# Kernel optimization log

Hardware: AMD Instinct MI355X
Metric: run time of the kernel (lower is better)

The kernel has to match this reference:

```python
import jax, jax.numpy as jnp
import numpy as np
from jax import lax


def conv1x1(x, w, b):
    # x [B,Ci,H,W], w [Co,Ci], b [Co]
    return jnp.einsum('oi,bihw->bohw', w, x) + b[None, :, None, None]


def dil_conv_relu(x, w, b):
    # 3x3 conv, dilation 2, padding 2 (make_layers with dilation=True), then ReLU
    y = lax.conv_general_dilated(x, w, (1, 1), [(2, 2), (2, 2)], rhs_dilation=(2, 2),
                                 dimension_numbers=('NCHW', 'OIHW', 'NCHW'))
    return jax.nn.relu(y + b[None, :, None, None])


def conv1d_relu(x, w, b):
    # x [n,c,L], w [o,i,9], padding 4 -> same length; conv + ReLU (nn.Sequential(Conv2d, ReLU))
    y = lax.conv_general_dilated(x, w, (1,), [(4, 4)], dimension_numbers=('NCH', 'OIH', 'NCH'))
    return jax.nn.relu(y + b[None, :, None])


def dulr_pass(slices, w, b):
    # slices [L,n,c,m]; out[0]=slices[0]; out[i]=convrelu(out[i-1]) + slices[i]
    def step(carry, s):
        new = conv1d_relu(carry, w, b) + s
        return new, new
    _, rest = lax.scan(step, slices[0], slices[1:])
    return jnp.concatenate([slices[:1], rest], axis=0)


def conv_du(x, w, b):
    # down pass then up pass over rows (kernel (1,9) -> 1D conv along width)
    rows = jnp.moveaxis(x, 2, 0)            # [h,n,c,w]
    rows = dulr_pass(rows, w, b)
    rows = dulr_pass(rows[::-1], w, b)[::-1]
    return jnp.moveaxis(rows, 0, 2)


def conv_lr(x, w, b):
    # left-right then right-left over columns (kernel (9,1) -> 1D conv along height)
    cols = jnp.moveaxis(x, 3, 0)            # [w,n,c,h]
    cols = dulr_pass(cols, w, b)
    cols = dulr_pass(cols[::-1], w, b)[::-1]
    return jnp.moveaxis(cols, 0, 3)


def setup_inputs() -> dict:
    key = jax.random.key(0)
    ks = jax.random.split(key, 24)
    B, H, W = 4, 64, 64
    std = 0.01
    f32 = jnp.float32
    d = {}
    d['in_data'] = jax.random.normal(ks[0], (B, 1025, H, W), f32)
    d['wA'] = jax.random.normal(ks[1], (128, 1024), f32) * std
    d['bA'] = jax.random.normal(ks[2], (128,), f32) * std
    d['wB'] = jax.random.normal(ks[3], (128, 1024), f32) * std
    d['bB'] = jax.random.normal(ks[4], (128,), f32) * std
    d['wC'] = jax.random.normal(ks[5], (1024, 1024), f32) * std
    d['bC'] = jax.random.normal(ks[6], (1024,), f32) * std
    d['gamma'] = jnp.array(0.1, f32)
    chans = [(512, 1024), (512, 512), (512, 512), (256, 512), (128, 256), (64, 128)]
    for i, (co, ci) in enumerate(chans):
        d[f'bw{i+1}'] = jax.random.normal(ks[7 + 2 * i], (co, ci, 3, 3), f32) * std
        d[f'bb{i+1}'] = jax.random.normal(ks[8 + 2 * i], (co,), f32) * std
    d['du_w'] = jax.random.normal(ks[19], (64, 64, 9), f32) * std
    d['du_b'] = jax.random.normal(ks[20], (64,), f32) * std
    d['lr_w'] = jax.random.normal(ks[21], (64, 64, 9), f32) * std
    d['lr_b'] = jax.random.normal(ks[22], (64,), f32) * std
    d['ow'] = jax.random.normal(ks[23], (1, 64), f32) * std
    d['ob'] = jnp.zeros((1,), f32)
    return d


def reference(in_data, wA, bA, wB, bB, wC, bC, gamma,
              bw1, bb1, bw2, bb2, bw3, bb3, bw4, bb4, bw5, bb5, bw6, bb6,
              du_w, du_b, lr_w, lr_b, ow, ob):
    x = in_data[:, :1024]                   # [B,1024,H,W]
    f = in_data[:, 1024:1025]               # [B,1,H,W]
    B, C, H, W = x.shape
    N = H * W
    # appearance_A(x) -> query [B,128,N]
    q = conv1x1(x, wA, bA).reshape(B, 128, N)
    # f1024 = f broadcast to 1024 channels; flow_B(f1024) (1x1 conv) == f * sum_i wB[:,i] + bB
    k = (f * wB.sum(axis=1)[None, :, None, None] + bB[None, :, None, None]).reshape(B, 128, N)
    energy = jnp.einsum('bcn,bcm->bnm', q, k)           # [B,N,N] = q^T k
    att = jax.nn.softmax(energy, axis=-1)
    v = conv1x1(x, wC, bC).reshape(B, C, N)             # appearance_C
    out = jnp.einsum('bcj,bij->bci', v, att).reshape(B, C, H, W)  # bmm(v, att^T)
    x = gamma * out + x
    for w_, b_ in ((bw1, bb1), (bw2, bb2), (bw3, bb3), (bw4, bb4), (bw5, bb5), (bw6, bb6)):
        x = dil_conv_relu(x, w_, b_)
    x = conv_du(x, du_w, du_b)
    x = conv_lr(x, lr_w, lr_b)
    x = jax.nn.relu(conv1x1(x, ow, ob))                 # o_layer
    # F.upsample(scale_factor=8) default nearest
    x = jnp.repeat(jnp.repeat(x, 8, axis=2), 8, axis=3)
    return x
```

## Files before the change

kernel.cpp:

```cpp
#include <hip/hip_runtime.h>


#define NPIX 4096

typedef _Float16 f16;
typedef _Float16 f16x8 __attribute__((ext_vector_type(8)));
typedef _Float16 f16x4 __attribute__((ext_vector_type(4)));
typedef float f32x4 __attribute__((ext_vector_type(4)));

__device__ inline void async16(const void* g, void* l) {
  __builtin_amdgcn_global_load_lds(
      (const __attribute__((address_space(1))) unsigned int*)g,
      (__attribute__((address_space(3))) unsigned int*)l, 16, 0, 0);
}


__global__ void rf_zero(float* __restrict__ z) { z[threadIdx.x] = 0.f; }

__global__ void rf_s(const float* __restrict__ wB, const float* __restrict__ bA,
                     float* __restrict__ s_out, float* __restrict__ c0_out) {
  int c = threadIdx.x;
  const float* row = wB + (size_t)c * 1024;
  float acc = 0.f;
  for (int i = 0; i < 1024; ++i) acc += row[i];
  s_out[c] = acc;
  __shared__ float sh[128];
  sh[c] = acc * bA[c];
  __syncthreads();
  for (int off = 64; off > 0; off >>= 1) {
    if (c < off) sh[c] += sh[c + off];
    __syncthreads();
  }
  if (c == 0) c0_out[0] = sh[0];
}

__global__ void rf_u(const float* __restrict__ wA, const float* __restrict__ s,
                     float* __restrict__ u) {
  int i = blockIdx.x * 256 + threadIdx.x;
  float acc = 0.f;
  for (int c = 0; c < 128; ++c) acc += s[c] * wA[(size_t)c * 1024 + i];
  u[i] = acc;
}

__global__ void rf_fstat(const float* __restrict__ in, float* __restrict__ fstat) {
  int b = blockIdx.x;
  int t = threadIdx.x;
  const float* f = in + ((size_t)b * 1025 + 1024) * NPIX;
  float mx = -1e30f, mn = 1e30f;
  for (int j = t; j < NPIX; j += 256) {
    float v = f[j];
    mx = fmaxf(mx, v);
    mn = fminf(mn, v);
  }
  __shared__ float smx[256], smn[256];
  smx[t] = mx; smn[t] = mn;
  __syncthreads();
  for (int off = 128; off > 0; off >>= 1) {
    if (t < off) {
      smx[t] = fmaxf(smx[t], smx[t + off]);
      smn[t] = fminf(smn[t], smn[t + off]);
    }
    __syncthreads();
  }
  if (t == 0) { fstat[b] = smx[0]; fstat[4 + b] = smn[0]; }
}

__global__ __launch_bounds__(256) void rf_A(const float* __restrict__ in,
                                            const float* __restrict__ u,
                                            const float* __restrict__ c0p,
                                            const float* __restrict__ fst,
                                            float* __restrict__ A, float* __restrict__ M) {
  __shared__ float ul[1024];
  int b = blockIdx.y;
  int n = blockIdx.x * 256 + threadIdx.x;
  for (int s = threadIdx.x; s < 1024; s += 256) ul[s] = u[s];
  __syncthreads();
  const float* xp = in + (size_t)b * 1025 * NPIX + n;
  float acc = c0p[0];
#pragma unroll 8
  for (int i = 0; i < 1024; ++i) acc = fmaf(ul[i], xp[(size_t)i * NPIX], acc);
  A[b * NPIX + n] = acc;
  M[b * NPIX + n] = fmaxf(acc * fst[b], acc * fst[4 + b]);
}

__global__ void rf_Z(const float* __restrict__ in, const float* __restrict__ A,
                     const float* __restrict__ M, float* __restrict__ iZ) {
  int idx = blockIdx.x * 4 + (threadIdx.x >> 6);
  int lane = threadIdx.x & 63;
  int b = idx >> 12;
  const float* f = in + ((size_t)b * 1025 + 1024) * NPIX;
  float a = A[idx], m = M[idx];
  float acc = 0.f;
#pragma unroll 4
  for (int it = 0; it < 64; ++it) acc += __expf(a * f[lane + it * 64] - m);
  for (int off = 32; off > 0; off >>= 1) acc += __shfl_down(acc, off, 64);
  if (lane == 0) iZ[idx] = 1.0f / acc;
}


__global__ void rf_xsplit(const float* __restrict__ in, f16* __restrict__ xh) {
  __shared__ float tl[64][65];
  int nt = blockIdx.x, ct = blockIdx.y, b = blockIdx.z;
  int n0 = nt * 64, c0 = ct * 64;
  int tid = threadIdx.x;
  for (int s = tid; s < 4096; s += 256) {
    int r = s >> 6, c = s & 63;
    tl[r][c] = in[((size_t)b * 1025 + c0 + r) * NPIX + n0 + c];
  }
  __syncthreads();
  for (int s = tid; s < 512; s += 256) {
    int n = s >> 3, g = s & 7;
    f16x8 hb;
#pragma unroll
    for (int q = 0; q < 8; ++q) hb[q] = (f16)(16.f * tl[g * 8 + q][n]);
    size_t o = (((size_t)b * 128 + (c0 >> 3) + g) * 4096 + n0 + n) * 8;
    *(f16x8*)&xh[o] = hb;
  }
}


__global__ void rf_wC1(const float* __restrict__ wC, f16* __restrict__ wh) {
  int base = (blockIdx.x * 256 + threadIdx.x) * 8;
  int c = base >> 10, i0 = base & 1023;
  f16x8 hb;
#pragma unroll
  for (int q = 0; q < 8; ++q) hb[q] = (f16)(256.f * wC[base + q]);
  *(f16x8*)&wh[(((size_t)(i0 >> 3)) * 1024 + c) * 8] = hb;
}


__global__ __launch_bounds__(256, 2) void rf_vgemmm(
    const f16* __restrict__ wh, const f16* __restrict__ xh,
    const float* __restrict__ bC, f16* __restrict__ vH) {
  __shared__ f16 sA[2][4096], sB[2][4096];
  const int tid = threadIdx.x;
  const int nb = blockIdx.x * 128, cb = blockIdx.y * 128, b = blockIdx.z;
  const int pA = tid & 127;
  const int wv = tid >> 6, lane = tid & 63;
  const int mrow = lane & 15, quad = lane >> 4;
  const int wm = (wv & 1) * 64, wn = (wv >> 1) * 64;
  f32x4 acc[4][4];
#pragma unroll
  for (int i = 0; i < 4; ++i)
#pragma unroll
    for (int j = 0; j < 4; ++j) acc[i][j] = (f32x4){0.f, 0.f, 0.f, 0.f};

  auto stage = [&](int k0, int pb) {
    const int kg = k0 >> 3;
#pragma unroll
    for (int s = 0; s < 2; ++s) {
      const int cc = ((tid + 256 * s) >> 7) & 3;
      const int lb = ((tid & ~63) + 256 * s) * 8;
      async16(wh + ((size_t)(kg + cc) * 1024 + cb + pA) * 8, &sA[pb][lb]);
      async16(xh + (((size_t)b * 128 + kg + cc) * 4096 + nb + pA) * 8, &sB[pb][lb]);
    }
  };
  stage(0, 0);
  int p = 0;
  for (int k0 = 0; k0 < 1024; k0 += 32) {
    __syncthreads();
    if (k0 + 32 < 1024) stage(k0 + 32, p ^ 1);
    f16x8 fa[4], fb[4];
#pragma unroll
    for (int mi = 0; mi < 4; ++mi)
      fa[mi] = *(const f16x8*)&sA[p][(quad * 128 + wm + mi * 16 + mrow) * 8];
#pragma unroll
    for (int ni = 0; ni < 4; ++ni)
      fb[ni] = *(const f16x8*)&sB[p][(quad * 128 + wn + ni * 16 + mrow) * 8];
#pragma unroll
    for (int mi = 0; mi < 4; ++mi)
#pragma unroll
      for (int ni = 0; ni < 4; ++ni)
        acc[mi][ni] = __builtin_amdgcn_mfma_f32_16x16x32_f16(fa[mi], fb[ni], acc[mi][ni], 0, 0, 0);
    p ^= 1;
  }
  const float inv = 1.0f / 4096.0f;
#pragma unroll
  for (int mi = 0; mi < 4; ++mi) {
#pragma unroll
    for (int rg = 0; rg < 4; ++rg) {
      int c = cb + wm + mi * 16 + quad * 4 + rg;
      float bv = bC[c];
#pragma unroll
      for (int ni = 0; ni < 4; ++ni) {
        int j = nb + wn + ni * 16 + mrow;
        vH[(((size_t)b * 512 + (j >> 3)) * 1024 + c) * 8 + (j & 7)] =
            (f16)(16.f * (acc[mi][ni][rg] * inv + bv));
      }
    }
  }
}


__global__ __launch_bounds__(256, 2) void rf_attm(
    const f16* __restrict__ vH,
    const float* __restrict__ Aarr, const float* __restrict__ Marr,
    const float* __restrict__ iZ, const float* __restrict__ in,
    const float* __restrict__ gptr, f16* __restrict__ yH) {
  __shared__ f16 sAh[3][8192];
  __shared__ f16 sPh[2][4096];
  __shared__ float fl[4096];
  const int tid = threadIdx.x;
  const int ib = blockIdx.x * 128, cb = blockIdx.y * 256, b = blockIdx.z;
  const int wv = tid >> 6, lane = tid & 63;
  const int mrow = lane & 15, quad = lane >> 4;
  const int wm = wv * 64;
  const int ni_ = tid & 127;
  const int kc0 = tid >> 7;
  const float av2 = Aarr[b * NPIX + ib + ni_] * 1.44269504f;
  const float mv2 = Marr[b * NPIX + ib + ni_] * 1.44269504f;
  const float* f = in + ((size_t)b * 1025 + 1024) * NPIX;
  const f16* vbase = vH + (size_t)b * 4194304 + ((size_t)cb + tid) * 8;

  f32x4 acc[4][8];
#pragma unroll
  for (int i = 0; i < 4; ++i)
#pragma unroll
    for (int j = 0; j < 8; ++j) acc[i][j] = (f32x4){0.f, 0.f, 0.f, 0.f};

  auto stage = [&](int j0, int pb) {
    const int jg = j0 >> 3;
#pragma unroll
    for (int s = 0; s < 4; ++s)
      async16(vbase + (size_t)(jg + s) * 8192, &sAh[pb][(s * 256 + tid) * 8]);
  };
  auto doP = [&](int j0, int pb) {
#pragma unroll
    for (int it = 0; it < 2; ++it) {
      const int kc = kc0 + 2 * it;
      const float4 fa4 = *(const float4*)&fl[j0 + kc * 8];
      const float4 fb4 = *(const float4*)&fl[j0 + kc * 8 + 4];
      const float fj[8] = {fa4.x, fa4.y, fa4.z, fa4.w, fb4.x, fb4.y, fb4.z, fb4.w};
      f16x8 ph;
#pragma unroll
      for (int q = 0; q < 8; ++q)
        ph[q] = (f16)exp2f(fmaf(av2, fj[q], -mv2));
      *(f16x8*)&sPh[pb][(kc * 128 + ni_) * 8] = ph;
    }
  };

#pragma unroll
  for (int s = 0; s < 4; ++s)
    async16(f + (tid + 256 * s) * 4, &fl[((tid & ~63) + 256 * s) * 4]);
  stage(0, 0);
  asm volatile("s_waitcnt vmcnt(0)" ::: "memory");
  __builtin_amdgcn_s_barrier();
  doP(0, 0);
  stage(32, 1);
  asm volatile("s_waitcnt lgkmcnt(0)" ::: "memory");
  __builtin_amdgcn_s_barrier();

  for (int k = 0; k < 126; ++k) {
    const int pa = k % 3;
    const int pp = k & 1;
    f16x8 fa[4], fb[8];
#pragma unroll
    for (int mi = 0; mi < 4; ++mi)
      fa[mi] = *(const f16x8*)&sAh[pa][(quad * 256 + wm + mi * 16 + mrow) * 8];
#pragma unroll
    for (int ni = 0; ni < 8; ++ni)
      fb[ni] = *(const f16x8*)&sPh[pp][(quad * 128 + ni * 16 + mrow) * 8];
    stage((k + 2) * 32, (k + 2) % 3);
    doP((k + 1) * 32, pp ^ 1);
#pragma unroll
    for (int mi = 0; mi < 4; ++mi)
#pragma unroll
      for (int ni = 0; ni < 8; ++ni)
        acc[mi][ni] = __builtin_amdgcn_mfma_f32_16x16x32_f16(fa[mi], fb[ni], acc[mi][ni], 0, 0, 0);
    asm volatile("s_waitcnt vmcnt(4) lgkmcnt(0)" ::: "memory");
    __builtin_amdgcn_s_barrier();
  }
  {
    f16x8 fa[4], fb[8];
#pragma unroll
    for (int mi = 0; mi < 4; ++mi)
      fa[mi] = *(const f16x8*)&sAh[0][(quad * 256 + wm + mi * 16 + mrow) * 8];
#pragma unroll
    for (int ni = 0; ni < 8; ++ni)
      fb[ni] = *(const f16x8*)&sPh[0][(quad * 128 + ni * 16 + mrow) * 8];
    doP(127 * 32, 1);
#pragma unroll
    for (int mi = 0; mi < 4; ++mi)
#pragma unroll
      for (int ni = 0; ni < 8; ++ni)
        acc[mi][ni] = __builtin_amdgcn_mfma_f32_16x16x32_f16(fa[mi], fb[ni], acc[mi][ni], 0, 0, 0);
    asm volatile("s_waitcnt vmcnt(0) lgkmcnt(0)" ::: "memory");
    __builtin_amdgcn_s_barrier();
  }
  {
    f16x8 fa[4], fb[8];
#pragma unroll
    for (int mi = 0; mi < 4; ++mi)
      fa[mi] = *(const f16x8*)&sAh[1][(quad * 256 + wm + mi * 16 + mrow) * 8];
#pragma unroll
    for (int ni = 0; ni < 8; ++ni)
      fb[ni] = *(const f16x8*)&sPh[1][(quad * 128 + ni * 16 + mrow) * 8];
#pragma unroll
    for (int mi = 0; mi < 4; ++mi)
#pragma unroll
      for (int ni = 0; ni < 8; ++ni)
        acc[mi][ni] = __builtin_amdgcn_mfma_f32_16x16x32_f16(fa[mi], fb[ni], acc[mi][ni], 0, 0, 0);
  }

  const float g = gptr[0];
  const float inv16 = 1.0f / 16.0f;
  float zvi[8];
#pragma unroll
  for (int ni = 0; ni < 8; ++ni)
    zvi[ni] = iZ[b * NPIX + ib + ni * 16 + mrow] * inv16;
#pragma unroll
  for (int mi = 0; mi < 4; ++mi) {
    const int cbase = cb + wm + mi * 16 + quad * 4;
#pragma unroll
    for (int ni = 0; ni < 8; ++ni) {
      const int i = ib + ni * 16 + mrow;
      f16x4 hv;
#pragma unroll
      for (int rg = 0; rg < 4; ++rg) {
        float xr = in[((size_t)b * 1025 + cbase + rg) * NPIX + i];
        hv[rg] = (f16)(16.f * (g * (acc[mi][ni][rg] * zvi[ni]) + xr));
      }
      *(f16x4*)&yH[(((size_t)b * 128 + (cbase >> 3)) * 4096 + i) * 8 + (cbase & 7)] = hv;
    }
  }
}


__global__ void rf_wfragc(const float* __restrict__ w, f16* __restrict__ F,
                          int CI, int CO) {
  int gid = blockIdx.x * 256 + threadIdx.x;
  const int C16 = CO >> 4, KI = CI >> 5;
  const int total = 9 * KI * C16 * 64;
  if (gid >= total) return;
  int lane = gid & 63;
  int rest = gid >> 6;
  int c16 = rest % C16;
  int rest2 = rest / C16;
  int k = rest2 % KI;
  int t = rest2 / KI;
  int co = c16 * 16 + (lane & 15);
  int ci = k * 32 + (lane >> 4) * 8;
  f16x8 hb;
#pragma unroll
  for (int j = 0; j < 8; ++j)
    hb[j] = (f16)(256.0f * w[((size_t)co * CI + ci + j) * 9 + t]);
  *(f16x8*)&F[(size_t)gid * 8] = hb;
}


template <int BM, int BN, bool F32OUT>
__global__ __launch_bounds__(256, 2) void rf_mconv(
    const f16* __restrict__ xh, const f16* __restrict__ F,
    const float* __restrict__ bias, const float* __restrict__ zp,
    f16* __restrict__ oh, float* __restrict__ of, int CI, int CO) {
  constexpr int ROWS = BM / 64;
  constexpr int TPI = 4096 / BM;
  constexpr int HROWS = ROWS + 4;
  constexpr int COLP = 72;
  constexpr int CHUNKS = HROWS * 4 * COLP;
  constexpr int NSTG = (CHUNKS + 255) / 256;
  __shared__ f16 sA[2][NSTG * 2048];
  const int tid = threadIdx.x;
  const int blkpx = blockIdx.x;
  const int cob = blockIdx.y * BN;
  const int b = blkpx / TPI;
  const int h0 = (blkpx - b * TPI) * ROWS;

  const int wv = tid >> 6, lane = tid & 63;
  const int mrow = lane & 15, quad = lane >> 4;
  const int wm = (BN == 128) ? (wv & 1) * 64 : wv * 64;
  const int wn = (BN == 128) ? (wv >> 1) * 64 : 0;
  const int r_out = wm >> 6;
  const int KI = CI >> 5;
  const int C16 = CO >> 4;
  const int cb16 = (cob + wn) >> 4;

  f32x4 acc[4][4];
#pragma unroll
  for (int i = 0; i < 4; ++i)
#pragma unroll
    for (int j = 0; j < 4; ++j) acc[i][j] = (f32x4){0.f, 0.f, 0.f, 0.f};

  const f16* abase[NSTG];
  unsigned vmask = 0;
#pragma unroll
  for (int s = 0; s < NSTG; ++s) {
    int idx = tid + 256 * s;
    int rowks = idx / COLP;
    int col = idx - rowks * COLP;
    int r = rowks >> 2, ks = rowks & 3;
    int srow = h0 + r - 2, scol = col - 2;
    bool ok = (idx < CHUNKS) && ((unsigned)srow < 64u) && ((unsigned)scol < 64u);
    abase[s] = ok ? xh + (((size_t)b * (CI >> 3) + ks) * 4096 + srow * 64 + scol) * 8
                  : (const f16*)zp;
    if (ok) vmask |= (1u << s);
  }
  auto stageA = [&](int k, int pb) {
#pragma unroll
    for (int s = 0; s < NSTG; ++s) {
      const f16* sp = abase[s] + (((vmask >> s) & 1u) ? k * 131072 : 0);
      async16(sp, &sA[pb][((tid & ~63) + 256 * s) * 8]);
    }
  };

  const f16* Fb = F + ((size_t)cb16 * 64 + lane) * 8;
  auto loadFB = [&](f16x8* dst, int t, int k) {
#pragma unroll
    for (int ni = 0; ni < 4; ++ni)
      dst[ni] = *(const f16x8*)(Fb + ((size_t)(t * KI + k) * C16 + ni) * 512);
  };

  stageA(0, 0);
  f16x8 fb0[4], fb1[4];
  loadFB(fb0, 0, 0);

  for (int k2 = 0; k2 < KI; k2 += 2) {
#pragma unroll
    for (int dk = 0; dk < 2; ++dk) {
      const int k = k2 + dk;
      __syncthreads();
#pragma unroll
      for (int t = 0; t < 9; ++t) {
        const int par = (t + dk) & 1;
        f16x8* cur = par ? fb1 : fb0;
        f16x8* nxt = par ? fb0 : fb1;
        if (t < 8) loadFB(nxt, t + 1, k);
        else if (k + 1 < KI) loadFB(nxt, 0, k + 1);
        const int dh = (t / 3) * 2 - 2, dw = (t - (t / 3) * 3) * 2 - 2;
        f16x8 fa[4];
#pragma unroll
        for (int mi = 0; mi < 4; ++mi)
          fa[mi] = *(const f16x8*)&sA[dk][(((r_out + dh + 2) * 4 + quad) * COLP +
                                          mi * 16 + mrow + dw + 2) * 8];
#pragma unroll
        for (int mi = 0; mi < 4; ++mi)
#pragma unroll
          for (int ni = 0; ni < 4; ++ni)
            acc[mi][ni] = __builtin_amdgcn_mfma_f32_16x16x32_f16(fa[mi], cur[ni], acc[mi][ni], 0, 0, 0);
      }
      if (k + 1 < KI) stageA(k + 1, dk ^ 1);
    }
  }

  const float inv = 1.0f / 4096.0f;
  float bvs[4];
#pragma unroll
  for (int ni = 0; ni < 4; ++ni) bvs[ni] = bias[cob + wn + ni * 16 + mrow];
#pragma unroll
  for (int mi = 0; mi < 4; ++mi) {
#pragma unroll
    for (int rg = 0; rg < 4; ++rg) {
      int px = wm + mi * 16 + quad * 4 + rg;
      int hh = h0 + (px >> 6), wwp = px & 63;
#pragma unroll
      for (int ni = 0; ni < 4; ++ni) {
        int co = cob + wn + ni * 16 + mrow;
        float vv = fmaxf(acc[mi][ni][rg] * inv + bvs[ni], 0.f);
        if (F32OUT) {
          of[(((size_t)b * CO + co) * 64 + hh) * 64 + wwp] = vv;
        } else {
          oh[(((size_t)b * (CO >> 3) + (co >> 3)) * 4096 + hh * 64 + wwp) * 8 + (co & 7)] =
              (f16)(vv * 16.f);
        }
      }
    }
  }
}


__global__ void rf_wfrag(const float* __restrict__ w, f16* __restrict__ fh) {
  int gid = blockIdx.x * 256 + threadIdx.x;
  if (gid >= 4608) return;
  int lane = gid & 63;
  int rem = gid >> 6;
  int kc = rem & 1;
  int rem2 = rem >> 1;
  int t = rem2 % 9;
  int w4 = rem2 / 9;
  int co = w4 * 16 + (lane & 15);
  int cib = kc * 32 + (lane >> 4) * 8;
  f16x8 hb;
#pragma unroll
  for (int j = 0; j < 8; ++j)
    hb[j] = (f16)(256.f * w[((size_t)co * 64 + cib + j) * 9 + t]);
  *(f16x8*)&fh[(size_t)gid * 8] = hb;
}


__global__ __launch_bounds__(256, 1) void rf_mscan(
    const float* __restrict__ src, float* __restrict__ dst,
    const f16* __restrict__ fh, const float* __restrict__ bias, int dir) {
  __shared__ f16 ch[72 * 64];
  const int b = blockIdx.x;
  const int tid = threadIdx.x;
  const int wave = tid >> 6, lane = tid & 63;
  const int quad = lane >> 4, l15 = lane & 15;

  f16x8 Ah[9][2];
#pragma unroll
  for (int t = 0; t < 9; ++t)
#pragma unroll
    for (int kc = 0; kc < 2; ++kc)
      Ah[t][kc] = *(const f16x8*)&fh[(((wave * 9 + t) * 2 + kc) * 64 + lane) * 8];
  float bvs[4];
#pragma unroll
  for (int r = 0; r < 4; ++r) bvs[r] = bias[wave * 16 + quad * 4 + r];

  for (int s = tid; s < 2304; s += 256) ((unsigned*)ch)[s] = 0u;
  __syncthreads();

  const size_t sbase = (size_t)b * 64 * 4096;
  const int row0 = (dir > 0) ? 0 : 63;
  {
    int pos0 = tid & 63, cig = tid >> 6;
#pragma unroll
    for (int q = 0; q < 16; ++q) {
      int ci = cig * 16 + q;
      float v = src[sbase + (size_t)ci * 4096 + row0 * 64 + pos0];
      dst[sbase + (size_t)ci * 4096 + row0 * 64 + pos0] = v;
      int rowIdx = pos0 + 4;
      ch[rowIdx * 64 + (((ci >> 3) ^ (rowIdx & 7)) << 3) + (ci & 7)] = (f16)v;
    }
  }
  __syncthreads();

  const float inv = 1.0f / 256.0f;
  for (int s = 1; s < 64; ++s) {
    const int row = (dir > 0) ? s : 63 - s;
    float srow[4][4];
#pragma unroll
    for (int nt = 0; nt < 4; ++nt)
#pragma unroll
      for (int r = 0; r < 4; ++r)
        srow[nt][r] = src[sbase + (size_t)(wave * 16 + quad * 4 + r) * 4096 +
                          row * 64 + nt * 16 + l15];
    f32x4 acc[4];
#pragma unroll
    for (int nt = 0; nt < 4; ++nt) acc[nt] = (f32x4){0.f, 0.f, 0.f, 0.f};
#pragma unroll
    for (int t = 0; t < 9; ++t)
#pragma unroll
      for (int kc = 0; kc < 2; ++kc) {
#pragma unroll
        for (int nt = 0; nt < 4; ++nt) {
          int rowIdx = nt * 16 + l15 + t;
          int gr = kc * 4 + quad;
          f16x8 Bh = *(const f16x8*)&ch[rowIdx * 64 + ((gr ^ (rowIdx & 7)) << 3)];
          acc[nt] = __builtin_amdgcn_mfma_f32_16x16x32_f16(Ah[t][kc], Bh, acc[nt], 0, 0, 0);
        }
      }
    __syncthreads();
#pragma unroll
    for (int nt = 0; nt < 4; ++nt) {
      int pos = nt * 16 + l15;
      int rowIdx = pos + 4;
      f16x4 hv;
#pragma unroll
      for (int r = 0; r < 4; ++r) {
        float v = fmaxf(acc[nt][r] * inv + bvs[r], 0.f) + srow[nt][r];
        dst[sbase + (size_t)(wave * 16 + quad * 4 + r) * 4096 + row * 64 + pos] = v;
        hv[r] = (f16)v;
      }
      int ci0 = wave * 16 + quad * 4;
      *(f16x4*)&ch[rowIdx * 64 + (((ci0 >> 3) ^ (rowIdx & 7)) << 3) + (ci0 & 7)] = hv;
    }
    __syncthreads();
  }
}


__global__ void rf_transpose(const float* __restrict__ src, float* __restrict__ dst) {
  int bc = blockIdx.x;
  __shared__ float tl[64][65];
  int tid = threadIdx.x;
  const float* sp = src + (size_t)bc * 4096;
  float* dp = dst + (size_t)bc * 4096;
  for (int s = tid; s < 4096; s += 256) {
    int h = s >> 6, w = s & 63;
    tl[w][h] = sp[s];
  }
  __syncthreads();
  for (int s = tid; s < 4096; s += 256) dp[s] = tl[s >> 6][s & 63];
}


__global__ void rf_final(const float* __restrict__ t, const float* __restrict__ ow,
                         const float* __restrict__ ob, float* __restrict__ out) {
  int b = blockIdx.y;
  int s = blockIdx.x * 256 + threadIdx.x;
  int w = s >> 6, h = s & 63;
  float acc = ob[0];
  for (int c = 0; c < 64; ++c)
    acc += ow[c] * t[(((size_t)b * 64 + c) * 64 + w) * 64 + h];
  acc = fmaxf(acc, 0.f);
  float4 vv = make_float4(acc, acc, acc, acc);
  for (int dy = 0; dy < 8; ++dy) {
    float* dp = out + ((size_t)b * 512 + h * 8 + dy) * 512 + w * 8;
    *(float4*)dp = vv;
    *(float4*)(dp + 4) = vv;
  }
}


extern "C" void kernel_launch(void* const* d_in, const int* in_sizes, int n_in,
                              void* d_out, int out_size, void* d_ws, size_t ws_size,
                              hipStream_t stream) {
  const float* in    = (const float*)d_in[0];
  const float* wA    = (const float*)d_in[1];
  const float* bA    = (const float*)d_in[2];
  const float* wB    = (const float*)d_in[3];
  const float* wC    = (const float*)d_in[5];
  const float* bC    = (const float*)d_in[6];
  const float* gamma = (const float*)d_in[7];
  const float* bw1 = (const float*)d_in[8];  const float* bb1 = (const float*)d_in[9];
  const float* bw2 = (const float*)d_in[10]; const float* bb2 = (const float*)d_in[11];
  const float* bw3 = (const float*)d_in[12]; const float* bb3 = (const float*)d_in[13];
  const float* bw4 = (const float*)d_in[14]; const float* bb4 = (const float*)d_in[15];
  const float* bw5 = (const float*)d_in[16]; const float* bb5 = (const float*)d_in[17];
  const float* bw6 = (const float*)d_in[18]; const float* bb6 = (const float*)d_in[19];
  const float* du_w = (const float*)d_in[20]; const float* du_b = (const float*)d_in[21];
  const float* lr_w = (const float*)d_in[22]; const float* lr_b = (const float*)d_in[23];
  const float* ow   = (const float*)d_in[24]; const float* ob   = (const float*)d_in[25];
  float* out = (float*)d_out;
  float* ws = (float*)d_ws;

  f16* vH  = (f16*)(ws + 0);
  f16* xTh = (f16*)(ws + 4194304);
  f16* wCh = (f16*)(ws + 8388608);
  f16* yH  = (f16*)(ws + 16777216);
  f16* w1h = (f16*)(ws + 0);
  f16* c1H = (f16*)(ws + 2359296);
  f16* w3h = (f16*)(ws + 6553600);
  f16* w2h = (f16*)(ws + 16777216);
  f16* c2H = (f16*)(ws + 17956864);
  f16* w4h = (f16*)(ws + 22151168);
  f16* c4H = (f16*)(ws + 22740992);
  f16* c3H = c1H;
  f16* w5h = (f16*)(ws + 0);
  f16* c5H = (f16*)(ws + 147456);
  f16* w6h = (f16*)(ws + 1196032);
  float* tin = ws + 1232896;
  float* t0  = ws + 2281472;
  float* t1  = ws + 3330048;
  f16* duFh = (f16*)(ws + 4378624);
  f16* lrFh = (f16*)(ws + 4397056);
  float* sm = ws + 33554432;
  float* A_  = sm;
  float* M_  = sm + 16384;
  float* iZ  = sm + 32768;
  float* u_  = sm + 49152;
  float* s_  = sm + 50176;
  float* c0_ = sm + 50304;
  float* fst = sm + 50308;
  float* zp  = sm + 50432;

  rf_zero<<<1, 64, 0, stream>>>(zp);
  rf_s<<<1, 128, 0, stream>>>(wB, bA, s_, c0_);
  rf_u<<<4, 256, 0, stream>>>(wA, s_, u_);
  rf_fstat<<<4, 256, 0, stream>>>(in, fst);
  rf_A<<<dim3(16, 4), 256, 0, stream>>>(in, u_, c0_, fst, A_, M_);
  rf_Z<<<4096, 256, 0, stream>>>(in, A_, M_, iZ);
  rf_xsplit<<<dim3(64, 16, 4), 256, 0, stream>>>(in, xTh);
  rf_wC1<<<512, 256, 0, stream>>>(wC, wCh);
  rf_vgemmm<<<dim3(32, 8, 4), 256, 0, stream>>>(wCh, xTh, bC, vH);
  rf_attm<<<dim3(32, 4, 4), 256, 0, stream>>>(vH, A_, M_, iZ, in, gamma, yH);

  rf_wfragc<<<2304, 256, 0, stream>>>(bw1, w1h, 1024, 512);
  rf_wfragc<<<1152, 256, 0, stream>>>(bw3, w3h, 512, 512);
  rf_mconv<128, 128, false><<<dim3(128, 4), 256, 0, stream>>>(
      yH, w1h, bb1, zp, c1H, nullptr, 1024, 512);
  rf_wfragc<<<1152, 256, 0, stream>>>(bw2, w2h, 512, 512);
  rf_wfragc<<<576, 256, 0, stream>>>(bw4, w4h, 512, 256);
  rf_wfragc<<<144, 256, 0, stream>>>(bw5, w5h, 256, 128);
  rf_wfragc<<<36, 256, 0, stream>>>(bw6, w6h, 128, 64);
  rf_mconv<128, 128, false><<<dim3(128, 4), 256, 0, stream>>>(
      c1H, w2h, bb2, zp, c2H, nullptr, 512, 512);
  rf_mconv<128, 128, false><<<dim3(128, 4), 256, 0, stream>>>(
      c2H, w3h, bb3, zp, c3H, nullptr, 512, 512);
  rf_mconv<128, 128, false><<<dim3(128, 2), 256, 0, stream>>>(
      c3H, w4h, bb4, zp, c4H, nullptr, 512, 256);
  rf_wfrag<<<18, 256, 0, stream>>>(du_w, duFh);
  rf_wfrag<<<18, 256, 0, stream>>>(lr_w, lrFh);
  rf_mconv<128, 128, false><<<dim3(128, 1), 256, 0, stream>>>(
      c4H, w5h, bb5, zp, c5H, nullptr, 256, 128);
  rf_mconv<256, 64, true><<<dim3(64, 1), 256, 0, stream>>>(
      c5H, w6h, bb6, zp, nullptr, tin, 128, 64);

  rf_mscan<<<4, 256, 0, stream>>>(tin, t0, duFh, du_b, +1);
  rf_mscan<<<4, 256, 0, stream>>>(t0, t1, duFh, du_b, -1);
  rf_transpose<<<256, 256, 0, stream>>>(t1, t0);
  rf_mscan<<<4, 256, 0, stream>>>(t0, t1, lrFh, lr_b, +1);
  rf_mscan<<<4, 256, 0, stream>>>(t1, t0, lrFh, lr_b, -1);
  rf_final<<<dim3(16, 4), 256, 0, stream>>>(t0, ow, ob, out);
}
```

Measured before the change: 1.556 ms.

## Double-buffer LDS row state and prefetch next skip row in scan kernel

The recurrent row-scan kernel now keeps two LDS buffers for the previous row's f16 state, so each step reads one buffer and writes the other. This removes one of the two block barriers per step. It also prefetches the next row's skip-connection values from global memory one iteration ahead, hiding load latency behind the MFMA work. The cost is twice the shared memory and extra registers for the prefetched values.

Result: faster. 1.465 ms (-5.9%).

```diff
diff --git a/kernel.cpp b/kernel.cpp
--- a/kernel.cpp
+++ b/kernel.cpp
@@ -490,7 +490,7 @@
 __global__ __launch_bounds__(256, 1) void rf_mscan(
     const float* __restrict__ src, float* __restrict__ dst,
     const f16* __restrict__ fh, const float* __restrict__ bias, int dir) {
-  __shared__ f16 ch[72 * 64];
+  __shared__ f16 ch[2][72 * 64];
   const int b = blockIdx.x;
   const int tid = threadIdx.x;
   const int wave = tid >> 6, lane = tid & 63;
@@ -506,7 +506,7 @@
 #pragma unroll
   for (int r = 0; r < 4; ++r) bvs[r] = bias[wave * 16 + quad * 4 + r];
 
-  for (int s = tid; s < 2304; s += 256) ((unsigned*)ch)[s] = 0u;
+  for (int s = tid; s < 4608; s += 256) ((unsigned*)ch)[s] = 0u;
   __syncthreads();
 
   const size_t sbase = (size_t)b * 64 * 4096;
@@ -519,21 +519,40 @@
       float v = src[sbase + (size_t)ci * 4096 + row0 * 64 + pos0];
       dst[sbase + (size_t)ci * 4096 + row0 * 64 + pos0] = v;
       int rowIdx = pos0 + 4;
-      ch[rowIdx * 64 + (((ci >> 3) ^ (rowIdx & 7)) << 3) + (ci & 7)] = (f16)v;
-    }
+      ch[0][rowIdx * 64 + (((ci >> 3) ^ (rowIdx & 7)) << 3) + (ci & 7)] = (f16)v;
+    }
+  }
+  float srN[4][4];
+  {
+    const int rown = (dir > 0) ? 1 : 62;
+#pragma unroll
+    for (int nt = 0; nt < 4; ++nt)
+#pragma unroll
+      for (int r = 0; r < 4; ++r)
+        srN[nt][r] = src[sbase + (size_t)(wave * 16 + quad * 4 + r) * 4096 +
+                         rown * 64 + nt * 16 + l15];
   }
   __syncthreads();
 
   const float inv = 1.0f / 256.0f;
   for (int s = 1; s < 64; ++s) {
     const int row = (dir > 0) ? s : 63 - s;
+    const f16* chp = ch[(s - 1) & 1];
+    f16* chw = ch[s & 1];
     float srow[4][4];
 #pragma unroll
     for (int nt = 0; nt < 4; ++nt)
 #pragma unroll
-      for (int r = 0; r < 4; ++r)
-        srow[nt][r] = src[sbase + (size_t)(wave * 16 + quad * 4 + r) * 4096 +
-                          row * 64 + nt * 16 + l15];
+      for (int r = 0; r < 4; ++r) srow[nt][r] = srN[nt][r];
+    if (s < 63) {
+      const int rown = (dir > 0) ? s + 1 : 63 - (s + 1);
+#pragma unroll
+      for (int nt = 0; nt < 4; ++nt)
+#pragma unroll
+        for (int r = 0; r < 4; ++r)
+          srN[nt][r] = src[sbase + (size_t)(wave * 16 + quad * 4 + r) * 4096 +
+                           rown * 64 + nt * 16 + l15];
+    }
     f32x4 acc[4];
 #pragma unroll
     for (int nt = 0; nt < 4; ++nt) acc[nt] = (f32x4){0.f, 0.f, 0.f, 0.f};
@@ -545,11 +564,10 @@
         for (int nt = 0; nt < 4; ++nt) {
           int rowIdx = nt * 16 + l15 + t;
           int gr = kc * 4 + quad;
-          f16x8 Bh = *(const f16x8*)&ch[rowIdx * 64 + ((gr ^ (rowIdx & 7)) << 3)];
+          f16x8 Bh = *(const f16x8*)&chp[rowIdx * 64 + ((gr ^ (rowIdx & 7)) << 3)];
           acc[nt] = __builtin_amdgcn_mfma_f32_16x16x32_f16(Ah[t][kc], Bh, acc[nt], 0, 0, 0);
         }
       }
-    __syncthreads();
 #pragma unroll
     for (int nt = 0; nt < 4; ++nt) {
       int pos = nt * 16 + l15;
@@ -562,7 +580,7 @@
         hv[r] = (f16)v;
       }
       int ci0 = wave * 16 + quad * 4;
-      *(f16x4*)&ch[rowIdx * 64 + (((ci0 >> 3) ^ (rowIdx & 7)) << 3) + (ci0 & 7)] = hv;
+      *(f16x4*)&chw[rowIdx * 64 + (((ci0 >> 3) ^ (rowIdx & 7)) << 3) + (ci0 & 7)] = hv;
     }
     __syncthreads();
   }
```
